# Kernel optimization log

Hardware: AMD Instinct MI355X
Metric: run time of the kernel (lower is better)

The kernel has to match this reference:

```python
import jax, jax.numpy as jnp
import numpy as np

D_MODEL = 2048
N_Q = 16
N_KV = 4
HEAD_DIM = 128
WINDOW = 512
ROPE_BASE = 10000.0


def _rope_cos_sin(T, dtype):
    half = HEAD_DIM // 2
    inv_freq = 1.0 / (ROPE_BASE ** (jnp.arange(0, half, dtype=jnp.float32) * 2.0 / HEAD_DIM))
    pos = jnp.arange(T, dtype=jnp.float32)
    ang = pos[:, None] * inv_freq[None, :]            # [T, half]
    emb = jnp.concatenate([ang, ang], axis=-1)        # [T, HEAD_DIM]
    return jnp.cos(emb).astype(dtype), jnp.sin(emb).astype(dtype)


def _rotate_half(x):
    x1, x2 = jnp.split(x, 2, axis=-1)
    return jnp.concatenate([-x2, x1], axis=-1)


def _apply_rope(t, cos, sin):
    # t: [B, H, T, hd]; cos/sin: [T, hd]
    return t * cos[None, None, :, :] + _rotate_half(t) * sin[None, None, :, :]


def setup_inputs() -> dict:
    key = jax.random.key(0)
    ks = jax.random.split(key, 5)
    s = 0.02
    return {
        "x": jax.random.normal(ks[0], (2, 2048, D_MODEL), dtype=jnp.float32),
        "wq": jax.random.normal(ks[1], (D_MODEL, N_Q * HEAD_DIM), dtype=jnp.float32) * s,
        "wk": jax.random.normal(ks[2], (D_MODEL, N_KV * HEAD_DIM), dtype=jnp.float32) * s,
        "wv": jax.random.normal(ks[3], (D_MODEL, N_KV * HEAD_DIM), dtype=jnp.float32) * s,
        "wo": jax.random.normal(ks[4], (N_Q * HEAD_DIM, D_MODEL), dtype=jnp.float32) * s,
    }


def reference(x, wq, wk, wv, wo):
    B, T, _ = x.shape
    q = (x @ wq).reshape(B, T, N_Q, HEAD_DIM).transpose(0, 2, 1, 3)    # [B,Hq,T,hd]
    k = (x @ wk).reshape(B, T, N_KV, HEAD_DIM).transpose(0, 2, 1, 3)   # [B,Hkv,T,hd]
    v = (x @ wv).reshape(B, T, N_KV, HEAD_DIM).transpose(0, 2, 1, 3)

    cos, sin = _rope_cos_sin(T, x.dtype)
    q = _apply_rope(q, cos, sin)
    k = _apply_rope(k, cos, sin)

    # GQA: repeat_interleave kv heads to match q heads
    g = N_Q // N_KV
    k = jnp.repeat(k, g, axis=1)
    v = jnp.repeat(v, g, axis=1)

    scale = 1.0 / np.sqrt(HEAD_DIM)
    scores = jnp.einsum("bhqd,bhkd->bhqk", q, k) * scale

    idx = jnp.arange(T)
    diff = idx[:, None] - idx[None, :]
    keep = (diff >= 0) & (diff < WINDOW)               # causal & sliding window
    scores = jnp.where(keep[None, None, :, :], scores, jnp.finfo(scores.dtype).min)
    attn = jax.nn.softmax(scores, axis=-1)

    out = jnp.einsum("bhqk,bhkd->bhqd", attn, v)       # [B,Hq,T,hd]
    out = out.transpose(0, 2, 1, 3).reshape(B, T, N_Q * HEAD_DIM)
    return out @ wo
```

## Files before the change

kernel.cpp:

```cpp
#include <hip/hip_runtime.h>

#define T_SEQ   2048
#define DM      2048
#define N_Q     16
#define N_KV    4
#define HD      128
#define WIN     512
#define NB      2
#define NQKV    3072
#define QK_SCALE_L2E 0.12751744f

typedef short bf16x8 __attribute__((ext_vector_type(8)));
typedef float f32x4  __attribute__((ext_vector_type(4)));
typedef float f32x16 __attribute__((ext_vector_type(16)));
typedef unsigned short us4v __attribute__((ext_vector_type(4)));

__device__ __forceinline__ unsigned short f2bf(float f) {
    union { float f; unsigned u; } v; v.f = f;
    unsigned u = v.u;
    u += 0x7fffu + ((u >> 16) & 1u);
    return (unsigned short)(u >> 16);
}
__device__ __forceinline__ float bf2f(unsigned short h) {
    union { unsigned u; float f; } v; v.u = ((unsigned)h) << 16;
    return v.f;
}
__device__ __forceinline__ unsigned cvt_pk_bf16(float a, float b) {
    unsigned r;
    asm("v_cvt_pk_bf16_f32 %0, %1, %2" : "=v"(r) : "v"(a), "v"(b));
    return r;
}

#define GLOAD_LDS16(g, l) __builtin_amdgcn_global_load_lds( \
    (const __attribute__((address_space(1))) void*)(g),     \
    (__attribute__((address_space(3))) void*)(l), 16, 0, 0)

struct us4 { unsigned short a, b, c, d; };


__global__ __launch_bounds__(256)
void prep_a(const float* __restrict__ x, const float* __restrict__ wq,
            const float* __restrict__ wk, const float* __restrict__ wv,
            const float* __restrict__ wo,
            unsigned short* __restrict__ xbf, unsigned short* __restrict__ wqkvT,
            unsigned short* __restrict__ woT,
            float* __restrict__ cosT, float* __restrict__ sinT) {
    __shared__ float tile[32][33];
    int blk = blockIdx.x;
    if (blk < 8192) {
        long i = ((long)blk * 256 + threadIdx.x) * 4;
        float4 f = *(const float4*)(x + i);
        us4 o; o.a = f2bf(f.x); o.b = f2bf(f.y); o.c = f2bf(f.z); o.d = f2bf(f.w);
        *(us4*)(xbf + i) = o;
        return;
    }
    blk -= 8192;
    if (blk < 10240) {
        const float* in; unsigned short* outp; int C, bx, by;
        if (blk < 4096)      { in = wq; outp = wqkvT;                         C = DM;  bx = blk & 63;          by = blk >> 6; }
        else if (blk < 5120) { int k = blk - 4096; in = wk; outp = wqkvT + (long)DM * DM;         C = 512; bx = k & 15; by = k >> 4; }
        else if (blk < 6144) { int k = blk - 5120; in = wv; outp = wqkvT + (long)(DM + 512) * DM; C = 512; bx = k & 15; by = k >> 4; }
        else                 { int k = blk - 6144; in = wo; outp = woT;                           C = DM;  bx = k & 63; by = k >> 6; }
        const int c0 = bx * 32, r0 = by * 32;
        const int tx = threadIdx.x & 31, ty = threadIdx.x >> 5;
#pragma unroll
        for (int i = 0; i < 4; ++i)
            tile[ty + i * 8][tx] = in[(long)(r0 + ty + i * 8) * C + c0 + tx];
        __syncthreads();
#pragma unroll
        for (int i = 0; i < 4; ++i)
            outp[(long)(c0 + ty + i * 8) * DM + r0 + tx] = f2bf(tile[tx][ty + i * 8]);
        return;
    }
    blk -= 10240;
    const int idx = blk * 256 + threadIdx.x;
    const int t = idx >> 6, d = idx & 63;
    const float inv = __expf(-(float)d * (9.210340371976184f / 64.0f));
    const float ang = (float)t * inv;
    cosT[idx] = cosf(ang);
    sinT[idx] = sinf(ang);
}


__global__ __launch_bounds__(256)
void prep_b(unsigned short* __restrict__ qkv,
            const float* __restrict__ cosT, const float* __restrict__ sinT) {
    const int idx = blockIdx.x * 256 + threadIdx.x;
    const int d4 = (idx & 15) * 4;
    const int hh = (idx >> 4) % 20;
    const int row = idx / (16 * 20);
    const int t = row & (T_SEQ - 1);
    const int col = (hh < N_Q) ? hh * HD + d4 : DM + (hh - N_Q) * HD + d4;
    unsigned short* p = qkv + (long)row * NQKV + col;
    us4v a = *(const us4v*)p;
    us4v b = *(const us4v*)(p + 64);
    float4 c = *(const float4*)&cosT[t * 64 + d4];
    float4 s = *(const float4*)&sinT[t * 64 + d4];
    const float sc = (hh < N_Q) ? QK_SCALE_L2E : 1.0f;
    us4v o1, o2;
    const float cc[4] = { c.x, c.y, c.z, c.w }, ss[4] = { s.x, s.y, s.z, s.w };
#pragma unroll
    for (int i = 0; i < 4; ++i) {
        const float av = bf2f(a[i]), bv = bf2f(b[i]);
        o1[i] = f2bf((av * cc[i] - bv * ss[i]) * sc);
        o2[i] = f2bf((bv * cc[i] + av * ss[i]) * sc);
    }
    *(us4v*)p        = o1;
    *(us4v*)(p + 64) = o2;
}


template<int OUT_BF16>
__global__ __launch_bounds__(256)
void gemm_bt(const unsigned short* __restrict__ A,
             const unsigned short* __restrict__ Bt,
             void* __restrict__ Cvoid, int K, int ldc,
             unsigned short* __restrict__ vt) {
    __shared__ __align__(16) unsigned short sA[128 * 64];
    __shared__ __align__(16) unsigned short sB[128 * 64];
    const int tid = threadIdx.x;
    const int lane = tid & 63;
    const int wid = tid >> 6;
    const int wr = (wid >> 1) * 64, wc = (wid & 1) * 64;
    const int l5 = lane >> 5, l31 = lane & 31;

    const int gx = gridDim.x;
    const int nwg = gx * gridDim.y;
    int flat = blockIdx.y * gx + blockIdx.x;
    flat = (flat & 7) * (nwg >> 3) + (flat >> 3);
    const long Arow0 = (long)(flat / gx) * 128;
    const long Brow0 = (long)(flat % gx) * 128;

    f32x16 acc[2][2] = {};

    for (int kt = 0; kt < K; kt += 64) {
        __syncthreads();
#pragma unroll
        for (int n = 0; n < 4; ++n) {
            const int linb = n * 256 + wid * 64;
            const int lin  = linb + lane;
            const int row  = lin >> 3;
            const int sw   = (row ^ (row >> 3)) & 7;
            const int sc   = (lin & 7) ^ sw;
            const unsigned short* gA = A  + (Arow0 + row) * K + kt + sc * 8;
            const unsigned short* gB = Bt + (Brow0 + row) * K + kt + sc * 8;
            GLOAD_LDS16(gA, &sA[linb * 8]);
            GLOAD_LDS16(gB, &sB[linb * 8]);
        }
        __syncthreads();
#pragma unroll
        for (int kc = 0; kc < 4; ++kc) {
            bf16x8 av[2], bv[2];
#pragma unroll
            for (int t = 0; t < 2; ++t) {
                const int rowa = wr + t * 32 + l31;
                const int ca = (kc * 2 + l5) ^ ((rowa ^ (rowa >> 3)) & 7);
                av[t] = *(const bf16x8*)&sA[rowa * 64 + ca * 8];
                const int rowb = wc + t * 32 + l31;
                const int cb = (kc * 2 + l5) ^ ((rowb ^ (rowb >> 3)) & 7);
                bv[t] = *(const bf16x8*)&sB[rowb * 64 + cb * 8];
            }
#pragma unroll
            for (int ti = 0; ti < 2; ++ti)
#pragma unroll
                for (int tj = 0; tj < 2; ++tj)
                    acc[ti][tj] = __builtin_amdgcn_mfma_f32_32x32x16_bf16(av[ti], bv[tj], acc[ti][tj], 0, 0, 0);
        }
    }

    if (OUT_BF16) {
        const int hb = (int)(Brow0 >> 7);
        unsigned short* C = (unsigned short*)Cvoid;
        if (hb >= 20) {
            const long bb = Arow0 >> 11;
            const int hkv = hb - 20;
#pragma unroll
            for (int ti = 0; ti < 2; ++ti)
#pragma unroll
                for (int tj = 0; tj < 2; ++tj) {
                    const int d = wc + tj * 32 + l31;
                    unsigned short* vp = vt + ((bb * 4 + hkv) * 128 + d) * (long)T_SEQ;
#pragma unroll
                    for (int r = 0; r < 16; ++r) {
                        const int t = (int)((Arow0 + wr + ti * 32 + (r & 3) + 8 * (r >> 2) + 4 * l5) & (T_SEQ - 1));
                        vp[t] = f2bf(acc[ti][tj][r]);
                    }
                }
        } else {
#pragma unroll
            for (int ti = 0; ti < 2; ++ti)
#pragma unroll
                for (int tj = 0; tj < 2; ++tj)
#pragma unroll
                    for (int r = 0; r < 16; ++r) {
                        const long row = Arow0 + wr + ti * 32 + (r & 3) + 8 * (r >> 2) + 4 * l5;
                        const long col = Brow0 + wc + tj * 32 + l31;
                        C[row * ldc + col] = f2bf(acc[ti][tj][r]);
                    }
        }
    } else {
        float* C = (float*)Cvoid;
#pragma unroll
        for (int ti = 0; ti < 2; ++ti)
#pragma unroll
            for (int tj = 0; tj < 2; ++tj)
#pragma unroll
                for (int r = 0; r < 16; ++r) {
                    const long row = Arow0 + wr + ti * 32 + (r & 3) + 8 * (r >> 2) + 4 * l5;
                    const long col = Brow0 + wc + tj * 32 + l31;
                    C[row * ldc + col] = acc[ti][tj][r];
                }
    }
}


__global__ __launch_bounds__(512, 2)
void attn_kernel(const unsigned short* __restrict__ qkv,
                 const unsigned short* __restrict__ vt,
                 unsigned short* __restrict__ aout) {
    const int qt = blockIdx.x, hkv = blockIdx.y, b = blockIdx.z;
    const int tid = threadIdx.x, lane = tid & 63, w = tid >> 6;
    const int qh = hkv * 4 + (w & 3);
    const int qsub = w >> 2;
    const int q0w = qt * 64 + qsub * 32;
    const int lo = lane & 15, hi = lane >> 4;

    __shared__ __align__(16) unsigned short sK[2][64 * 128];
    __shared__ __align__(16) unsigned short sV[2][128 * 64];
    __shared__ __align__(16) unsigned short plds[8][32 * 64];
    unsigned short* pl = plds[w];

    bf16x8 qf2[2][4];
#pragma unroll
    for (int f = 0; f < 2; ++f) {
        const unsigned short* qp = qkv + (long)(b * T_SEQ + q0w + f * 16 + lo) * NQKV + qh * HD + hi * 8;
#pragma unroll
        for (int s = 0; s < 4; ++s) qf2[f][s] = *(const bf16x8*)(qp + s * 32);
    }

    f32x4 of[8][2] = {};
    float m_r[2] = { -1e30f, -1e30f };
    float s_r[2] = { 0.f, 0.f };

    int kstart = qt * 64 - (WIN - 1);
    if (kstart < 0) kstart = 0;
    kstart &= ~63;
    const int kend = qt * 64 + 63;

    const unsigned short* kbase = qkv + (long)b * T_SEQ * NQKV + DM + hkv * HD;
    const unsigned short* vbase = vt + (long)(b * N_KV + hkv) * HD * T_SEQ;

    int kr[2], kc[2], vr[2], vc[2];
#pragma unroll
    for (int u = 0; u < 2; ++u) {
        const int c = u * 512 + tid;
        kr[u] = c >> 4;  kc[u] = (c & 15) ^ (kr[u] & 7);
        vr[u] = c >> 3;  vc[u] = (c & 7) ^ (vr[u] & 7);
    }

#define STAGE(bf, kt_) do {                                                              \
    _Pragma("unroll")                                                                    \
    for (int u = 0; u < 2; ++u) {                                                        \
        const int dbase = (u * 512 + w * 64) * 8;                                        \
        GLOAD_LDS16(kbase + (long)((kt_) + kr[u]) * NQKV + kc[u] * 8, &sK[bf][dbase]);   \
        GLOAD_LDS16(vbase + (long)vr[u] * T_SEQ + (kt_) + vc[u] * 8, &sV[bf][dbase]);    \
    } } while (0)

    STAGE(0, kstart);
    asm volatile("s_waitcnt vmcnt(0)" ::: "memory");
    __syncthreads();

    int buf = 0;
    for (int kt = kstart; kt <= kend; kt += 64) {
        if (kt + 64 <= kend) STAGE(buf ^ 1, kt + 64);

        f32x4 sf[4][2] = {};
        __builtin_amdgcn_s_setprio(1);
#pragma unroll
        for (int n = 0; n < 4; ++n) {
            const int row = n * 16 + lo;
#pragma unroll
            for (int s = 0; s < 4; ++s) {
                const int c = (s * 4 + hi) ^ (row & 7);
                bf16x8 kf = *(const bf16x8*)&sK[buf][row * 128 + c * 8];
                sf[n][0] = __builtin_amdgcn_mfma_f32_16x16x32_bf16(kf, qf2[0][s], sf[n][0], 0, 0, 0);
                sf[n][1] = __builtin_amdgcn_mfma_f32_16x16x32_bf16(kf, qf2[1][s], sf[n][1], 0, 0, 0);
            }
        }
        __builtin_amdgcn_s_setprio(0);

        const bool nomask = ((kt + 63) <= q0w) && ((q0w + 31 - kt) < WIN);

        float pv[2][4][4];
        float mx[2] = { -1e30f, -1e30f };
        if (nomask) {
#pragma unroll
            for (int f = 0; f < 2; ++f)
#pragma unroll
                for (int n = 0; n < 4; ++n)
#pragma unroll
                    for (int r = 0; r < 4; ++r) {
                        pv[f][n][r] = sf[n][f][r];
                        mx[f] = fmaxf(mx[f], pv[f][n][r]);
                    }
        } else {
#pragma unroll
            for (int f = 0; f < 2; ++f) {
                const int q = q0w + f * 16 + lo;
#pragma unroll
                for (int n = 0; n < 4; ++n)
#pragma unroll
                    for (int r = 0; r < 4; ++r) {
                        const int d = q - (kt + n * 16 + hi * 4 + r);
                        pv[f][n][r] = (d >= 0 && d < WIN) ? sf[n][f][r] : -1e30f;
                        mx[f] = fmaxf(mx[f], pv[f][n][r]);
                    }
            }
        }
#pragma unroll
        for (int f = 0; f < 2; ++f) {
            mx[f] = fmaxf(mx[f], __shfl_xor(mx[f], 16));
            mx[f] = fmaxf(mx[f], __shfl_xor(mx[f], 32));
        }

        const bool ok = (mx[0] <= m_r[0] + 8.0f) && (mx[1] <= m_r[1] + 8.0f);
        if (!__all(ok)) {
#pragma unroll
            for (int f = 0; f < 2; ++f) {
                const float mnew = fmaxf(m_r[f], mx[f]);
                const float resc = exp2f(m_r[f] - mnew);
                s_r[f] *= resc;
                m_r[f] = mnew;
                float r4[4];
#pragma unroll
                for (int r = 0; r < 4; ++r) r4[r] = __shfl(resc, hi * 4 + r);
#pragma unroll
                for (int j = 0; j < 8; ++j) {
                    of[j][f][0] *= r4[0]; of[j][f][1] *= r4[1];
                    of[j][f][2] *= r4[2]; of[j][f][3] *= r4[3];
                }
            }
        }

#pragma unroll
        for (int f = 0; f < 2; ++f) {
            float psum = 0.f;
#pragma unroll
            for (int n = 0; n < 4; ++n)
#pragma unroll
                for (int r = 0; r < 4; ++r) {
                    pv[f][n][r] = exp2f(pv[f][n][r] - m_r[f]);
                    psum += pv[f][n][r];
                }
            psum += __shfl_xor(psum, 16);
            psum += __shfl_xor(psum, 32);
            s_r[f] += psum;
        }

        const int swz = (lo & 7) << 3;
#pragma unroll
        for (int f = 0; f < 2; ++f) {
            const int rowq = f * 16 + lo;
#pragma unroll
            for (int n = 0; n < 4; ++n) {
                const int k0 = n * 16 + hi * 4;
                *(unsigned*)&pl[rowq * 64 + (k0 ^ swz)]       = cvt_pk_bf16(pv[f][n][0], pv[f][n][1]);
                *(unsigned*)&pl[rowq * 64 + ((k0 + 2) ^ swz)] = cvt_pk_bf16(pv[f][n][2], pv[f][n][3]);
            }
        }
        asm volatile("s_waitcnt lgkmcnt(0)" ::: "memory");
        __builtin_amdgcn_sched_barrier(0);
        bf16x8 pa2[2][2];
#pragma unroll
        for (int f = 0; f < 2; ++f)
#pragma unroll
            for (int ks = 0; ks < 2; ++ks) {
                const int c = (ks * 4 + hi) ^ (lo & 7);
                pa2[f][ks] = *(const bf16x8*)&pl[(f * 16 + lo) * 64 + c * 8];
            }

        __builtin_amdgcn_s_setprio(1);
#pragma unroll
        for (int j = 0; j < 8; ++j) {
            const int row = j * 16 + lo;
#pragma unroll
            for (int ks = 0; ks < 2; ++ks) {
                const int c = (ks * 4 + hi) ^ (row & 7);
                bf16x8 vf = *(const bf16x8*)&sV[buf][row * 64 + c * 8];
                of[j][0] = __builtin_amdgcn_mfma_f32_16x16x32_bf16(pa2[0][ks], vf, of[j][0], 0, 0, 0);
                of[j][1] = __builtin_amdgcn_mfma_f32_16x16x32_bf16(pa2[1][ks], vf, of[j][1], 0, 0, 0);
            }
        }
        __builtin_amdgcn_s_setprio(0);

        asm volatile("s_waitcnt vmcnt(0)" ::: "memory");
        __syncthreads();
        buf ^= 1;
    }
#undef STAGE

#pragma unroll
    for (int f = 0; f < 2; ++f) {
        float s4[4];
#pragma unroll
        for (int r = 0; r < 4; ++r) s4[r] = __shfl(s_r[f], hi * 4 + r);
#pragma unroll
        for (int r = 0; r < 4; ++r) {
            const int qrow = q0w + f * 16 + hi * 4 + r;
            const float inv = 1.0f / s4[r];
            unsigned short* op = aout + (long)(b * T_SEQ + qrow) * DM + qh * HD + lo;
#pragma unroll
            for (int j = 0; j < 8; ++j) op[j * 16] = f2bf(of[j][f][r] * inv);
        }
    }
}


extern "C" void kernel_launch(void* const* d_in, const int* in_sizes, int n_in,
                              void* d_out, int out_size, void* d_ws, size_t ws_size,
                              hipStream_t stream) {
    (void)in_sizes; (void)n_in; (void)out_size; (void)ws_size;
    const float* x  = (const float*)d_in[0];
    const float* wq = (const float*)d_in[1];
    const float* wk = (const float*)d_in[2];
    const float* wv = (const float*)d_in[3];
    const float* wo = (const float*)d_in[4];
    float* out = (float*)d_out;
    char* ws = (char*)d_ws;

    unsigned short* xbf   = (unsigned short*)(ws);
    unsigned short* wqkvT = (unsigned short*)(ws + 16777216);
    unsigned short* woT   = (unsigned short*)(ws + 29360128);
    unsigned short* qkv   = (unsigned short*)(ws + 37748736);
    unsigned short* vt    = (unsigned short*)(ws + 62914560);
    unsigned short* aout  = (unsigned short*)(ws + 67108864);
    float* cosT = (float*)(ws + 83886080);
    float* sinT = (float*)(ws + 84410368);

    prep_a<<<dim3(18944), dim3(256), 0, stream>>>(x, wq, wk, wv, wo, xbf, wqkvT, woT, cosT, sinT);
    gemm_bt<1><<<dim3(NQKV / 128, 32), dim3(256), 0, stream>>>(xbf, wqkvT, qkv, DM, NQKV, vt);
    prep_b<<<dim3(5120), dim3(256), 0, stream>>>(qkv, cosT, sinT);
    attn_kernel<<<dim3(T_SEQ / 64, 4, 2), dim3(512), 0, stream>>>(qkv, vt, aout);
    gemm_bt<0><<<dim3(DM / 128, 32), dim3(256), 0, stream>>>(aout, woT, out, DM, DM, nullptr);
}
```

Before: 162.8 us.

## Fuse Q RoPE into attention and triple-buffer K/V staging

Q rotary embedding and the softmax scale are now applied inside the attention kernel on register-resident Q fragments, so prep_b only rotates K heads and launches far fewer blocks. The attention K/V shared-memory staging moves from double to triple buffering with a two-tile-ahead prefetch and partial vmcnt waits, replacing full waits and syncthreads with raw barriers. The goal is to remove a pass over Q in global memory and to hide load latency better. The cost is more LDS per block, which may reduce occupancy under launch_bounds(512,2), and redundant clamped loads at the tail.

```diff
diff --git a/kernel.cpp b/kernel.cpp
--- a/kernel.cpp
+++ b/kernel.cpp
@@ -87,23 +87,22 @@
             const float* __restrict__ cosT, const float* __restrict__ sinT) {
     const int idx = blockIdx.x * 256 + threadIdx.x;
     const int d4 = (idx & 15) * 4;
-    const int hh = (idx >> 4) % 20;
-    const int row = idx / (16 * 20);
+    const int hh = (idx >> 4) & 3;
+    const int row = idx >> 6;
     const int t = row & (T_SEQ - 1);
-    const int col = (hh < N_Q) ? hh * HD + d4 : DM + (hh - N_Q) * HD + d4;
+    const int col = DM + hh * HD + d4;
     unsigned short* p = qkv + (long)row * NQKV + col;
     us4v a = *(const us4v*)p;
     us4v b = *(const us4v*)(p + 64);
     float4 c = *(const float4*)&cosT[t * 64 + d4];
     float4 s = *(const float4*)&sinT[t * 64 + d4];
-    const float sc = (hh < N_Q) ? QK_SCALE_L2E : 1.0f;
     us4v o1, o2;
     const float cc[4] = { c.x, c.y, c.z, c.w }, ss[4] = { s.x, s.y, s.z, s.w };
 #pragma unroll
     for (int i = 0; i < 4; ++i) {
         const float av = bf2f(a[i]), bv = bf2f(b[i]);
-        o1[i] = f2bf((av * cc[i] - bv * ss[i]) * sc);
-        o2[i] = f2bf((bv * cc[i] + av * ss[i]) * sc);
+        o1[i] = f2bf(av * cc[i] - bv * ss[i]);
+        o2[i] = f2bf(bv * cc[i] + av * ss[i]);
     }
     *(us4v*)p        = o1;
     *(us4v*)(p + 64) = o2;
@@ -217,6 +216,7 @@
 __global__ __launch_bounds__(512, 2)
 void attn_kernel(const unsigned short* __restrict__ qkv,
                  const unsigned short* __restrict__ vt,
+                 const float* __restrict__ cosT, const float* __restrict__ sinT,
                  unsigned short* __restrict__ aout) {
     const int qt = blockIdx.x, hkv = blockIdx.y, b = blockIdx.z;
     const int tid = threadIdx.x, lane = tid & 63, w = tid >> 6;
@@ -225,8 +225,8 @@
     const int q0w = qt * 64 + qsub * 32;
     const int lo = lane & 15, hi = lane >> 4;
 
-    __shared__ __align__(16) unsigned short sK[2][64 * 128];
-    __shared__ __align__(16) unsigned short sV[2][128 * 64];
+    __shared__ __align__(16) unsigned short sK[3][64 * 128];
+    __shared__ __align__(16) unsigned short sV[3][128 * 64];
     __shared__ __align__(16) unsigned short plds[8][32 * 64];
     unsigned short* pl = plds[w];
 
@@ -236,6 +236,26 @@
         const unsigned short* qp = qkv + (long)(b * T_SEQ + q0w + f * 16 + lo) * NQKV + qh * HD + hi * 8;
 #pragma unroll
         for (int s = 0; s < 4; ++s) qf2[f][s] = *(const bf16x8*)(qp + s * 32);
+    }
+#pragma unroll
+    for (int f = 0; f < 2; ++f) {
+        const int t = q0w + f * 16 + lo;
+        const float* cb = cosT + t * 64 + hi * 8;
+        const float* sb = sinT + t * 64 + hi * 8;
+        float c0[8], s0[8], c1[8], s1[8];
+        *(float4*)&c0[0] = *(const float4*)cb;        *(float4*)&c0[4] = *(const float4*)(cb + 4);
+        *(float4*)&c1[0] = *(const float4*)(cb + 32); *(float4*)&c1[4] = *(const float4*)(cb + 36);
+        *(float4*)&s0[0] = *(const float4*)sb;        *(float4*)&s0[4] = *(const float4*)(sb + 4);
+        *(float4*)&s1[0] = *(const float4*)(sb + 32); *(float4*)&s1[4] = *(const float4*)(sb + 36);
+#pragma unroll
+        for (int j = 0; j < 8; ++j) {
+            const float a0 = bf2f(qf2[f][0][j]), a1 = bf2f(qf2[f][1][j]);
+            const float a2 = bf2f(qf2[f][2][j]), a3 = bf2f(qf2[f][3][j]);
+            qf2[f][0][j] = f2bf((a0 * c0[j] - a2 * s0[j]) * QK_SCALE_L2E);
+            qf2[f][2][j] = f2bf((a2 * c0[j] + a0 * s0[j]) * QK_SCALE_L2E);
+            qf2[f][1][j] = f2bf((a1 * c1[j] - a3 * s1[j]) * QK_SCALE_L2E);
+            qf2[f][3][j] = f2bf((a3 * c1[j] + a1 * s1[j]) * QK_SCALE_L2E);
+        }
     }
 
     f32x4 of[8][2] = {};
@@ -246,6 +266,7 @@
     if (kstart < 0) kstart = 0;
     kstart &= ~63;
     const int kend = qt * 64 + 63;
+    const int ktmax = T_SEQ - 64;
 
     const unsigned short* kbase = qkv + (long)b * T_SEQ * NQKV + DM + hkv * HD;
     const unsigned short* vbase = vt + (long)(b * N_KV + hkv) * HD * T_SEQ;
@@ -267,12 +288,18 @@
     } } while (0)
 
     STAGE(0, kstart);
-    asm volatile("s_waitcnt vmcnt(0)" ::: "memory");
-    __syncthreads();
-
-    int buf = 0;
+    {
+        int k1 = kstart + 64; if (k1 > ktmax) k1 = ktmax;
+        STAGE(1, k1);
+    }
+
+    int bufc = 0;
     for (int kt = kstart; kt <= kend; kt += 64) {
-        if (kt + 64 <= kend) STAGE(buf ^ 1, kt + 64);
+        int kt2 = kt + 128; if (kt2 > ktmax) kt2 = ktmax;
+        const int bs = (bufc + 2 >= 3) ? bufc - 1 : bufc + 2;
+        STAGE(bs, kt2);
+        asm volatile("s_waitcnt vmcnt(8)" ::: "memory");
+        __builtin_amdgcn_s_barrier();
 
         f32x4 sf[4][2] = {};
         __builtin_amdgcn_s_setprio(1);
@@ -282,7 +309,7 @@
 #pragma unroll
             for (int s = 0; s < 4; ++s) {
                 const int c = (s * 4 + hi) ^ (row & 7);
-                bf16x8 kf = *(const bf16x8*)&sK[buf][row * 128 + c * 8];
+                bf16x8 kf = *(const bf16x8*)&sK[bufc][row * 128 + c * 8];
                 sf[n][0] = __builtin_amdgcn_mfma_f32_16x16x32_bf16(kf, qf2[0][s], sf[n][0], 0, 0, 0);
                 sf[n][1] = __builtin_amdgcn_mfma_f32_16x16x32_bf16(kf, qf2[1][s], sf[n][1], 0, 0, 0);
             }
@@ -386,16 +413,15 @@
 #pragma unroll
             for (int ks = 0; ks < 2; ++ks) {
                 const int c = (ks * 4 + hi) ^ (row & 7);
-                bf16x8 vf = *(const bf16x8*)&sV[buf][row * 64 + c * 8];
+                bf16x8 vf = *(const bf16x8*)&sV[bufc][row * 64 + c * 8];
                 of[j][0] = __builtin_amdgcn_mfma_f32_16x16x32_bf16(pa2[0][ks], vf, of[j][0], 0, 0, 0);
                 of[j][1] = __builtin_amdgcn_mfma_f32_16x16x32_bf16(pa2[1][ks], vf, of[j][1], 0, 0, 0);
             }
         }
         __builtin_amdgcn_s_setprio(0);
 
-        asm volatile("s_waitcnt vmcnt(0)" ::: "memory");
-        __syncthreads();
-        buf ^= 1;
+        __builtin_amdgcn_s_barrier();
+        bufc = (bufc + 1 >= 3) ? 0 : bufc + 1;
     }
 #undef STAGE
 
@@ -439,7 +465,7 @@
 
     prep_a<<<dim3(18944), dim3(256), 0, stream>>>(x, wq, wk, wv, wo, xbf, wqkvT, woT, cosT, sinT);
     gemm_bt<1><<<dim3(NQKV / 128, 32), dim3(256), 0, stream>>>(xbf, wqkvT, qkv, DM, NQKV, vt);
-    prep_b<<<dim3(5120), dim3(256), 0, stream>>>(qkv, cosT, sinT);
-    attn_kernel<<<dim3(T_SEQ / 64, 4, 2), dim3(512), 0, stream>>>(qkv, vt, aout);
+    prep_b<<<dim3(1024), dim3(256), 0, stream>>>(qkv, cosT, sinT);
+    attn_kernel<<<dim3(T_SEQ / 64, 4, 2), dim3(512), 0, stream>>>(qkv, vt, cosT, sinT, aout);
     gemm_bt<0><<<dim3(DM / 128, 32), dim3(256), 0, stream>>>(aout, woT, out, DM, DM, nullptr);
 }
```

Result: no change. 162.8 us (-0.0%).
